# Optimization experiments

Measured on AMD Instinct MI355X. Metric: run time of the kernel, lower is better.

Reference implementation:

```python
import jax, jax.numpy as jnp
import numpy as np

GRID_SIZE = 5
G1 = GRID_SIZE + 1
GRID = jnp.linspace(-1.0, 1.0, G1)
INV2SIG2 = 0.5 * GRID_SIZE ** 2  # 1/(2*sigma^2), sigma = 1/grid_size
L = 3      # num_layers
NH = 8     # num_heads
C = 256    # feature_dim
HID = 1024 # hidden_dim


def kan(x, bw, sw):
    # x: (T, in), bw: (out, in), sw: (out, in, G1)
    base = x @ bw.T
    bases = jnp.exp(-((x[..., None] - GRID) ** 2) * INV2SIG2)  # (T, in, G1)
    bases = bases / (bases.sum(-1, keepdims=True) + 1e-8)
    return base + jnp.einsum('big,oig->bo', bases, sw)


def layernorm(x, g, b, eps=1e-5):
    m = x.mean(-1, keepdims=True)
    v = x.var(-1, keepdims=True)
    return (x - m) / jnp.sqrt(v + eps) * g + b


def gelu(x):
    return jax.nn.gelu(x, approximate=False)


def _forward(sat_features, uav_features,
             sat_qkvp_base, sat_qkvp_spline, sat_rp_base, sat_rp_spline,
             uav_qkvp_base, uav_qkvp_spline, uav_rp_base, uav_rp_spline,
             ref_w1_base, ref_w1_spline, ref_w2_base, ref_w2_spline, ref_ln_g, ref_ln_b,
             sim_w1_base, sim_w1_spline, sim_w2_base, sim_w2_spline, sim_w3_base, sim_w3_spline,
             fus_w_base, fus_w_spline, fus_ln_g, fus_ln_b):
    B, Cc, H, W = sat_features.shape
    N = H * W
    HD = Cc // NH
    scale = HD ** -0.5
    sat = sat_features.reshape(B, Cc, N).transpose(0, 2, 1)  # (B, N, C)
    uav = uav_features.reshape(B, Cc, N).transpose(0, 2, 1)

    # relative coords (same geometry every layer)
    ch = jnp.arange(H)
    cw = jnp.arange(W)
    coords = jnp.stack(jnp.meshgrid(ch, cw, indexing='ij')).reshape(2, N)  # (2, N)
    rel = (coords[:, :, None] - coords[:, None, :]).transpose(1, 2, 0).astype(jnp.float32)  # (N, N, 2)
    rel = rel / jnp.array([H - 1.0, W - 1.0], dtype=jnp.float32)
    rel_flat = rel.reshape(-1, 2)

    def attn_block(x, qb, qs, rb, rs):
        xf = x.reshape(-1, Cc)
        q = kan(xf, qb[0], qs[0]).reshape(B, N, NH, HD).transpose(0, 2, 1, 3)
        k = kan(xf, qb[1], qs[1]).reshape(B, N, NH, HD).transpose(0, 2, 1, 3)
        v = kan(xf, qb[2], qs[2]).reshape(B, N, NH, HD).transpose(0, 2, 1, 3)
        bias = kan(rel_flat, rb, rs).reshape(N, N, NH).transpose(2, 0, 1)  # (NH, N, N)
        a = jnp.einsum('bhnd,bhmd->bhnm', q, k) * scale + bias[None]
        a = jax.nn.softmax(a, axis=-1)
        o = jnp.einsum('bhnm,bhmd->bhnd', a, v).transpose(0, 2, 1, 3).reshape(B, N, Cc)
        return kan(o.reshape(-1, Cc), qb[3], qs[3]).reshape(B, N, Cc)

    def refine(x, i):
        xf = x.reshape(-1, Cc)
        h = gelu(kan(xf, ref_w1_base[i], ref_w1_spline[i]))
        h = kan(h, ref_w2_base[i], ref_w2_spline[i])
        h = layernorm(h, ref_ln_g[i], ref_ln_b[i])
        return h.reshape(x.shape)

    for i in range(L):
        se = attn_block(sat, sat_qkvp_base[i], sat_qkvp_spline[i], sat_rp_base[i], sat_rp_spline[i])
        ue = attn_block(uav, uav_qkvp_base[i], uav_qkvp_spline[i], uav_rp_base[i], uav_rp_spline[i])
        sat = se + refine(se, i)
        uav = ue + refine(ue, i)

    sg = sat.mean(1)  # (B, C)
    ug = uav.mean(1)
    si = jnp.concatenate([sg, ug], axis=1)
    h = gelu(kan(si, sim_w1_base, sim_w1_spline))
    h = gelu(kan(h, sim_w2_base, sim_w2_spline))
    w = jax.nn.sigmoid(kan(h, sim_w3_base, sim_w3_spline))  # (B, 1)
    fi = jnp.concatenate([sg * w, ug * (1.0 - w)], axis=1)
    out = gelu(layernorm(kan(fi, fus_w_base, fus_w_spline), fus_ln_g, fus_ln_b))
    return out


def setup_inputs() -> dict:
    key = jax.random.key(0)
    ks = jax.random.split(key, 32)
    B, H, W = 8, 24, 24
    n = lambda k, shape, s=0.05: jax.random.normal(k, shape, dtype=jnp.float32) * s
    inp = {
        'sat_features': jax.random.normal(ks[0], (B, C, H, W), dtype=jnp.float32),
        'uav_features': jax.random.normal(ks[1], (B, C, H, W), dtype=jnp.float32),
        'sat_qkvp_base': n(ks[2], (L, 4, C, C)),
        'sat_qkvp_spline': n(ks[3], (L, 4, C, C, G1), 0.01),
        'sat_rp_base': n(ks[4], (L, NH, 2)),
        'sat_rp_spline': n(ks[5], (L, NH, 2, G1), 0.01),
        'uav_qkvp_base': n(ks[6], (L, 4, C, C)),
        'uav_qkvp_spline': n(ks[7], (L, 4, C, C, G1), 0.01),
        'uav_rp_base': n(ks[8], (L, NH, 2)),
        'uav_rp_spline': n(ks[9], (L, NH, 2, G1), 0.01),
        'ref_w1_base': n(ks[10], (L, HID, C)),
        'ref_w1_spline': n(ks[11], (L, HID, C, G1), 0.01),
        'ref_w2_base': n(ks[12], (L, C, HID)),
        'ref_w2_spline': n(ks[13], (L, C, HID, G1), 0.01),
        'ref_ln_g': jnp.ones((L, C), jnp.float32),
        'ref_ln_b': jnp.zeros((L, C), jnp.float32),
        'sim_w1_base': n(ks[14], (HID, 2 * C)),
        'sim_w1_spline': n(ks[15], (HID, 2 * C, G1), 0.01),
        'sim_w2_base': n(ks[16], (C // 4, HID)),
        'sim_w2_spline': n(ks[17], (C // 4, HID, G1), 0.01),
        'sim_w3_base': n(ks[18], (1, C // 4)),
        'sim_w3_spline': n(ks[19], (1, C // 4, G1), 0.01),
        'fus_w_base': n(ks[20], (C, 2 * C)),
        'fus_w_spline': n(ks[21], (C, 2 * C, G1), 0.01),
        'fus_ln_g': jnp.ones((C,), jnp.float32),
        'fus_ln_b': jnp.zeros((C,), jnp.float32),
    }
    return inp


def reference(sat_features, uav_features,
              sat_qkvp_base, sat_qkvp_spline, sat_rp_base, sat_rp_spline,
              uav_qkvp_base, uav_qkvp_spline, uav_rp_base, uav_rp_spline,
              ref_w1_base, ref_w1_spline, ref_w2_base, ref_w2_spline, ref_ln_g, ref_ln_b,
              sim_w1_base, sim_w1_spline, sim_w2_base, sim_w2_spline, sim_w3_base, sim_w3_spline,
              fus_w_base, fus_w_spline, fus_ln_g, fus_ln_b):
    return _forward(sat_features, uav_features,
                    sat_qkvp_base, sat_qkvp_spline, sat_rp_base, sat_rp_spline,
                    uav_qkvp_base, uav_qkvp_spline, uav_rp_base, uav_rp_spline,
                    ref_w1_base, ref_w1_spline, ref_w2_base, ref_w2_spline, ref_ln_g, ref_ln_b,
                    sim_w1_base, sim_w1_spline, sim_w2_base, sim_w2_spline, sim_w3_base, sim_w3_spline,
                    fus_w_base, fus_w_spline, fus_ln_g, fus_ln_b)
```

## Files before the change

### kernel.cpp

```cpp
#include <hip/hip_runtime.h>
#include <math.h>

#define TT      4608
#define BB      8
#define NTOK    576
#define CDIM    256
#define NHEADS  8
#define HIDDIM  1024

typedef __attribute__((ext_vector_type(8))) short bf8s;
typedef __attribute__((ext_vector_type(4))) float f4;
typedef __attribute__((ext_vector_type(4))) short sv4;
typedef __attribute__((ext_vector_type(8))) short sv8;

__device__ __forceinline__ f4 mfma16(bf8s a, bf8s b, f4 c) {
    return __builtin_amdgcn_mfma_f32_16x16x32_bf16(a, b, c, 0, 0, 0);
}

__device__ __forceinline__ unsigned short f2bf(float x) {
    union { float f; unsigned int u; } v; v.f = x;
    unsigned int r = v.u + 0x7FFFu + ((v.u >> 16) & 1u);
    return (unsigned short)(r >> 16);
}
__device__ __forceinline__ float bf2f(unsigned short h) {
    union { unsigned int u; float f; } v; v.u = ((unsigned int)h) << 16;
    return v.f;
}
__device__ __forceinline__ unsigned int cvtpk(float a, float b) {
    unsigned int r;
    asm("v_cvt_pk_bf16_f32 %0, %1, %2" : "=v"(r) : "v"(a), "v"(b));
    return r;
}

__device__ __forceinline__ float gelu_f(float x) {
    return 0.5f * x * (1.0f + erff(x * 0.70710678118654752f));
}

__device__ __forceinline__ void bases6(float v, float* out) {
    float vc = fminf(fmaxf(v, -1.6f), 1.6f);
    float t = fmaf(vc, 10.f, 10.f);
    float r = __expf(t);
    float e0 = 1.f;
    float e1 = r * 1.3533528e-1f;
    float e2 = e1 * (r * 2.4787522e-3f);
    float e3 = e2 * (r * 4.5399930e-5f);
    float e4 = e3 * (r * 8.3152872e-7f);
    float e5 = e4 * (r * 1.5229979e-8f);
    float av = fmaxf(fabsf(v) - 1.f, 0.f);
    float g = __expf(fminf(fmaf(av * av, 12.5f, -18.420681f), 80.f));
    float inv = 1.f / ((e0 + e1 + e2 + e3 + e4 + e5) * (1.f + g));
    out[0] = e0 * inv; out[1] = e1 * inv; out[2] = e2 * inv;
    out[3] = e3 * inv; out[4] = e4 * inv; out[5] = e5 * inv;
}

__device__ __forceinline__ int4 expand_pack(float v) {
    float b6[6]; bases6(v, b6);
    int4 pk;
    pk.x = (int)cvtpk(v, b6[0]);
    pk.y = (int)cvtpk(b6[1], b6[2]);
    pk.z = (int)cvtpk(b6[3], b6[4]);
    pk.w = (int)cvtpk(b6[5], 0.f);
    return pk;
}

__device__ __forceinline__ void gload16(const void* g, void* l) {
    __builtin_amdgcn_global_load_lds(
        (const __attribute__((address_space(1))) unsigned int*)g,
        (__attribute__((address_space(3))) unsigned int*)l, 16, 0, 0);
}

__global__ __launch_bounds__(256) void k_transpose(const float* __restrict__ in,
                                                   float* __restrict__ out) {
    int idx = blockIdx.x * 256 + threadIdx.x;
    if (idx >= TT * CDIM) return;
    int t = idx >> 8, c = idx & 255;
    int b = t / NTOK, n = t % NTOK;
    out[idx] = in[(b * CDIM + c) * NTOK + n];
}

__global__ __launch_bounds__(256) void k_reduceS(const float4* __restrict__ p,
                                                 float4* __restrict__ out, int n4, int S) {
    int i = blockIdx.x * 256 + threadIdx.x;
    if (i >= n4) return;
    float4 a = p[i];
    for (int s = 1; s < S; s++) {
        float4 v = p[i + (size_t)s * n4];
        a.x += v.x; a.y += v.y; a.z += v.z; a.w += v.w;
    }
    out[i] = a;
}

__global__ __launch_bounds__(256) void k_reduce_exp(const float4* __restrict__ p,
                                                    float4* __restrict__ seb,
                                                    unsigned short* __restrict__ aexp,
                                                    int n4, int S) {
    int i = blockIdx.x * 256 + threadIdx.x;
    if (i >= n4) return;
    float4 a = p[i];
    for (int s = 1; s < S; s++) {
        float4 v = p[i + (size_t)s * n4];
        a.x += v.x; a.y += v.y; a.z += v.z; a.w += v.w;
    }
    seb[i] = a;
    int t = i >> 6, i4 = (i & 63) << 2;
    float xa[4] = {a.x, a.y, a.z, a.w};
#pragma unroll
    for (int u = 0; u < 4; u++) {
        int4 pk = expand_pack(xa[u]);
        *(int4*)(aexp + (size_t)t * 2048 + (size_t)(i4 + u) * 8) = pk;
    }
}

__global__ __launch_bounds__(256) void k_expand8(const float* __restrict__ x,
                                                 unsigned short* __restrict__ out, int Mr) {
    int idx = blockIdx.x * 256 + threadIdx.x;
    if (idx >= Mr * 64) return;
    int t = idx >> 6, i4 = (idx & 63) << 2;
    float4 xv = *(const float4*)(x + (size_t)t * 256 + i4);
    float xa[4] = {xv.x, xv.y, xv.z, xv.w};
#pragma unroll
    for (int u = 0; u < 4; u++) {
        int4 pk = expand_pack(xa[u]);
        *(int4*)(out + (size_t)t * 2048 + (size_t)(i4 + u) * 8) = pk;
    }
}

__global__ __launch_bounds__(256) void k_pack8(
    const float* __restrict__ sqb, const float* __restrict__ sqs,
    const float* __restrict__ uqb, const float* __restrict__ uqs,
    const float* __restrict__ w1b, const float* __restrict__ w1s,
    const float* __restrict__ w2b, const float* __restrict__ w2s,
    unsigned short* __restrict__ Wq, unsigned short* __restrict__ Wp,
    unsigned short* __restrict__ Ww1, unsigned short* __restrict__ Ww2) {
    const size_t gQ = 196608, gP = 65536, g1 = 262144;
    size_t idx = (size_t)blockIdx.x * 256 + threadIdx.x;
    const float* base; const float* spl; unsigned short* dst; size_t off;
    if (idx < 2 * gQ) {
        int s = idx >= gQ; off = idx - (size_t)s * gQ;
        base = s ? uqb : sqb; spl = s ? uqs : sqs; dst = Wq + (size_t)s * gQ * 8;
    } else if (idx < 2 * gQ + 2 * gP) {
        size_t o2 = idx - 2 * gQ; int s = o2 >= gP; off = o2 - (size_t)s * gP;
        base = (s ? uqb : sqb) + 3 * 65536; spl = (s ? uqs : sqs) + 3 * 393216;
        dst = Wp + (size_t)s * gP * 8;
    } else if (idx < 2 * gQ + 2 * gP + g1) {
        off = idx - 2 * gQ - 2 * gP; base = w1b; spl = w1s; dst = Ww1;
    } else {
        off = idx - 2 * gQ - 2 * gP - g1; base = w2b; spl = w2s; dst = Ww2;
    }
    float bv = base[off];
    float2 s01 = *(const float2*)(spl + off * 6);
    float2 s23 = *(const float2*)(spl + off * 6 + 2);
    float2 s45 = *(const float2*)(spl + off * 6 + 4);
    int4 pk;
    pk.x = (int)cvtpk(bv, s01.x);
    pk.y = (int)cvtpk(s01.y, s23.x);
    pk.z = (int)cvtpk(s23.y, s45.x);
    pk.w = (int)cvtpk(s45.y, 0.f);
    *(int4*)(dst + off * 8) = pk;
}

template<int BM, int BN, int ACT, int CMODE, int EXP>
__global__ __launch_bounds__(256) void mgemm(const void* __restrict__ Araw,
                                             const unsigned short* __restrict__ W0,
                                             const unsigned short* __restrict__ W1,
                                             void* __restrict__ Cv, int NN, int K,
                                             int ALD, int WLD, int gx, int groupRows,
                                             int S, int Kc, size_t skStride) {
    constexpr int MF = BM / 32;
    constexpr int NF = BN / 32;
    __shared__ unsigned short As[2][BM * 32];
    __shared__ unsigned short Bs[2][BN * 32];
    int nwg = gridDim.x, orig = blockIdx.x;
    int q = nwg >> 3, r = nwg & 7;
    int xcd = orig & 7, loc = orig >> 3;
    int wg = (xcd < r ? xcd * (q + 1) : r * (q + 1) + (xcd - r) * q) + loc;
    int sk = wg % S; int rest = wg / S;
    int bx = rest % gx, by = rest / gx;
    const int bm = by * BM, bn = bx * BN;
    const unsigned short* W = (bm >= groupRows) ? W1 : W0;
    const int tid = threadIdx.x, l = tid & 63, w = tid >> 6;
    const int wr = w >> 1, wc = w & 1;
    const int sr = l >> 2;
    const int scg = (l & 3) ^ ((l >> 3) & 3);
    const int sc8 = scg * 8;
    const int fro = (l & 15) * 32 + (((l >> 4) ^ ((l >> 1) & 3)) << 3);
    const int k0 = sk * Kc;
    f4 acc[MF][NF];
#pragma unroll
    for (int m = 0; m < MF; m++)
#pragma unroll
        for (int n = 0; n < NF; n++) acc[m][n] = (f4){0.f, 0.f, 0.f, 0.f};

    const unsigned short* Abf = (const unsigned short*)Araw;
    float xv[BM / 64];
    auto loadX = [&](int kt) {
#pragma unroll
        for (int it = 0; it < BM / 64; it++) {
            int ch = it * 4 + w;
            int row = bm + ch * 16 + sr;
            int xi = (kt >> 3) + scg;
            xv[it] = bf2f(Abf[(size_t)row * ALD + xi]);
        }
    };
    auto writeA = [&](int buf) {
#pragma unroll
        for (int it = 0; it < BM / 64; it++) {
            int ch = it * 4 + w;
            int4 pk = expand_pack(xv[it]);
            *(int4*)&As[buf][ch * 512 + l * 8] = pk;
        }
    };
    auto stageA = [&](int buf, int kt) {
#pragma unroll
        for (int it = 0; it < BM / 64; it++) {
            int ch = it * 4 + w;
            gload16(Abf + (size_t)(bm + ch * 16 + sr) * ALD + kt + sc8,
                    (void*)(&As[buf][ch * 512 + l * 8]));
        }
    };
    auto stageB = [&](int buf, int kt) {
#pragma unroll
        for (int it = 0; it < BN / 64; it++) {
            int ch = it * 4 + w;
            gload16(W + (size_t)(bn + ch * 16 + sr) * WLD + kt + sc8,
                    (void*)(&Bs[buf][ch * 512 + l * 8]));
        }
    };

    if constexpr (EXP == 0) stageA(0, k0);
    else { loadX(k0); writeA(0); }
    stageB(0, k0);
    __syncthreads();
    const int nt = Kc / 32;
    for (int t = 0; t < nt; t++) {
        int cur = t & 1;
        if (t + 1 < nt) {
            if constexpr (EXP == 0) stageA(cur ^ 1, k0 + (t + 1) * 32);
            else loadX(k0 + (t + 1) * 32);
            stageB(cur ^ 1, k0 + (t + 1) * 32);
        }
        bf8s af[MF], bfr[NF];
#pragma unroll
        for (int m = 0; m < MF; m++)
            af[m] = *(const bf8s*)&As[cur][(wr * MF + m) * 512 + fro];
#pragma unroll
        for (int n = 0; n < NF; n++)
            bfr[n] = *(const bf8s*)&Bs[cur][(wc * NF + n) * 512 + fro];
#pragma unroll
        for (int m = 0; m < MF; m++)
#pragma unroll
            for (int n = 0; n < NF; n++)
                acc[m][n] = mfma16(af[m], bfr[n], acc[m][n]);
        if constexpr (EXP != 0) { if (t + 1 < nt) writeA(cur ^ 1); }
        __syncthreads();
    }
#pragma unroll
    for (int m = 0; m < MF; m++)
#pragma unroll
        for (int n = 0; n < NF; n++)
#pragma unroll
            for (int j = 0; j < 4; j++) {
                int row = bm + wr * (BM / 2) + m * 16 + (l >> 4) * 4 + j;
                int col = bn + wc * (BN / 2) + n * 16 + (l & 15);
                float v = acc[m][n][j];
                if (ACT == 1) v = gelu_f(v);
                size_t o = (size_t)row * NN + col;
                if (CMODE == 0)      ((float*)Cv)[(size_t)sk * skStride + o] = v;
                else                 ((unsigned short*)Cv)[o] = f2bf(v);
            }
}

__global__ __launch_bounds__(256) void k_vt(const unsigned short* __restrict__ QKV,
                                            unsigned short* __restrict__ VT) {
    const int n0 = blockIdx.x * 64, h = blockIdx.y, z = blockIdx.z;
    __shared__ unsigned short t[32][72];
    const int tid = threadIdx.x;
    {
        int nl = tid >> 2, d8 = (tid & 3) * 8;
        sv8 v = *(const sv8*)(QKV + ((size_t)z * 576 + n0 + nl) * 768 + 512 + h * 32 + d8);
#pragma unroll
        for (int j = 0; j < 8; j++) t[d8 + j][nl] = v[j];
    }
    __syncthreads();
    {
        int d = tid >> 3, n8 = (tid & 7) * 8;
        sv8 o;
#pragma unroll
        for (int j = 0; j < 8; j++) o[j] = t[d][n8 + j];
        *(sv8*)(VT + ((size_t)(z * 8 + h) * 32 + d) * 576 + n0 + n8) = o;
    }
}

__global__ __launch_bounds__(256) void k_bias_tab(const float* __restrict__ rb0,
                                                  const float* __restrict__ rs0,
                                                  const float* __restrict__ rb1,
                                                  const float* __restrict__ rs1,
                                                  float* __restrict__ Btab) {
    int sidx = blockIdx.y;
    const float* rb = sidx ? rb1 : rb0;
    const float* rs = sidx ? rs1 : rs0;
    float* B = Btab + (size_t)sidx * NHEADS * 2209;
    int idx = blockIdx.x * 256 + threadIdx.x;
    if (idx >= 2209) return;
    float r0 = (float)(idx / 47 - 23) * (1.0f / 23.0f);
    float r1 = (float)(idx % 47 - 23) * (1.0f / 23.0f);
    float v[2][6];
    bases6(r0, v[0]);
    bases6(r1, v[1]);
#pragma unroll
    for (int h = 0; h < NHEADS; h++) {
        float s = rb[h * 2] * r0 + rb[h * 2 + 1] * r1;
#pragma unroll
        for (int g = 0; g < 6; g++)
            s += rs[h * 12 + g] * v[0][g] + rs[h * 12 + 6 + g] * v[1][g];
        B[(size_t)h * 2209 + idx] = s;
    }
}

__global__ __launch_bounds__(256) void k_attn2(const unsigned short* __restrict__ QKV,
                                               const unsigned short* __restrict__ VT,
                                               const float* __restrict__ Btab,
                                               unsigned short* __restrict__ AX) {
    int nwg = gridDim.x, orig = blockIdx.x;
    int qq = nwg >> 3, rr_ = nwg & 7;
    int xcd = orig & 7, loc = orig >> 3;
    int wg = (xcd < rr_ ? xcd * (qq + 1) : rr_ * (qq + 1) + (xcd - rr_) * qq) + loc;
    const int n0 = (wg % 18) * 32;
    const int h = (wg / 18) & 7;
    const int z = wg / 144;
    const int tid = threadIdx.x, l = tid & 63, w = tid >> 6;
    const int rh = (w & 1) * 16;
    const int kh = (w >> 1) * 16;
    __shared__ unsigned short Ps[4][32 * 40];
    __shared__ float red[4][16];
    __shared__ float bt[2209];
    const float scale = 0.17677669529663687f;
    const size_t rowbase = (size_t)z * NTOK;
    const float* Bh = Btab + ((size_t)(z >> 3) * NHEADS + h) * 2209;
    for (int i = tid; i < 2209; i += 256) bt[i] = Bh[i];
    const unsigned short* VTh = VT + ((size_t)(z * 8 + h) * 32) * 576;

    bf8s qf = *(const bf8s*)(QKV + (rowbase + n0 + rh + (l & 15)) * 768 + h * 32 + (l >> 4) * 8);

    f4 s[18];
#pragma unroll
    for (int kc = 0; kc < 18; kc++) {
        bf8s kf = *(const bf8s*)(QKV + (rowbase + kc * 32 + kh + (l & 15)) * 768 + 256 + h * 32 + (l >> 4) * 8);
        f4 zz = {0.f, 0.f, 0.f, 0.f};
        s[kc] = mfma16(qf, kf, zz);
    }
    __syncthreads();

    const int r0 = n0 + rh + (l >> 4) * 4;
    int bidx[4];
#pragma unroll
    for (int j = 0; j < 4; j++) {
        int n = r0 + j;
        bidx[j] = (n / 24 + 23) * 47 + (n % 24 + 23);
    }
    int m0 = kh + (l & 15);
    int mq = (m0 >= 24) ? 1 : 0;
    int mr = m0 - 24 * mq;
    float mx[4] = {-1e30f, -1e30f, -1e30f, -1e30f};
#pragma unroll
    for (int kc = 0; kc < 18; kc++) {
        int moff = mq * 47 + mr;
        mr += 8; mq += 1;
        if (mr >= 24) { mr -= 24; mq += 1; }
#pragma unroll
        for (int j = 0; j < 4; j++) {
            float v = s[kc][j] * scale + bt[bidx[j] - moff];
            s[kc][j] = v;
            mx[j] = fmaxf(mx[j], v);
        }
    }
#pragma unroll
    for (int j = 0; j < 4; j++)
#pragma unroll
        for (int m = 1; m < 16; m <<= 1) mx[j] = fmaxf(mx[j], __shfl_xor(mx[j], m));
    if ((l & 15) == 0) {
#pragma unroll
        for (int j = 0; j < 4; j++) red[w][(l >> 4) * 4 + j] = mx[j];
    }
    __syncthreads();
#pragma unroll
    for (int j = 0; j < 4; j++) mx[j] = fmaxf(mx[j], red[w ^ 2][(l >> 4) * 4 + j]);
    __syncthreads();
    float sm[4] = {0.f, 0.f, 0.f, 0.f};
#pragma unroll
    for (int kc = 0; kc < 18; kc++)
#pragma unroll
        for (int j = 0; j < 4; j++) {
            float p = __expf(s[kc][j] - mx[j]);
            s[kc][j] = p;
            sm[j] += p;
        }
#pragma unroll
    for (int j = 0; j < 4; j++)
#pragma unroll
        for (int m = 1; m < 16; m <<= 1) sm[j] += __shfl_xor(sm[j], m);
    if ((l & 15) == 0) {
#pragma unroll
        for (int j = 0; j < 4; j++) red[w][(l >> 4) * 4 + j] = sm[j];
    }
    __syncthreads();
#pragma unroll
    for (int j = 0; j < 4; j++) sm[j] = 1.f / (sm[j] + red[w ^ 2][(l >> 4) * 4 + j]);

    f4 oacc = {0.f, 0.f, 0.f, 0.f};
#pragma unroll
    for (int kc2 = 0; kc2 < 18; kc2 += 2) {
        const int b0 = kc2 & 2;
#pragma unroll
        for (int u = 0; u < 2; u++) {
            int kc = kc2 + u;
#pragma unroll
            for (int j = 0; j < 4; j++)
                Ps[b0 + u][(rh + (l >> 4) * 4 + j) * 40 + kh + (l & 15)] = f2bf(s[kc][j]);
        }
        __syncthreads();
#pragma unroll
        for (int u = 0; u < 2; u++) {
            int kc = kc2 + u;
            bf8s pf = *(const bf8s*)&Ps[b0 + u][(rh + (l & 15)) * 40 + (l >> 4) * 8];
            bf8s vf = *(const bf8s*)(VTh + (size_t)(kh + (l & 15)) * 576 + kc * 32 + (l >> 4) * 8);
            oacc = mfma16(pf, vf, oacc);
        }
    }
#pragma unroll
    for (int j = 0; j < 4; j++) {
        float ov = oacc[j] * sm[j];
        int4 pk = expand_pack(ov);
        *(int4*)(AX + ((rowbase + n0 + rh + (l >> 4) * 4 + j) * 2048
                       + (size_t)(h * 32 + kh + (l & 15)) * 8)) = pk;
    }
}

__global__ __launch_bounds__(256) void k_ln_addS(const float* __restrict__ P,
                                                 int S, size_t st,
                                                 const float* __restrict__ SE,
                                                 const float* __restrict__ g,
                                                 const float* __restrict__ bb,
                                                 float* __restrict__ Out,
                                                 unsigned short* __restrict__ aexp,
                                                 int doExp) {
    int t = blockIdx.x, c = threadIdx.x;
    size_t o = (size_t)t * 256 + c;
    float v = 0.f;
    for (int s = 0; s < S; s++) v += P[o + (size_t)s * st];
    float s1 = v, s2 = v * v;
#pragma unroll
    for (int off = 32; off; off >>= 1) { s1 += __shfl_xor(s1, off); s2 += __shfl_xor(s2, off); }
    __shared__ float p1[4], p2[4];
    int wv_ = c >> 6, ln = c & 63;
    if (ln == 0) { p1[wv_] = s1; p2[wv_] = s2; }
    __syncthreads();
    s1 = p1[0] + p1[1] + p1[2] + p1[3];
    s2 = p2[0] + p2[1] + p2[2] + p2[3];
    float m = s1 * (1.f / 256.f);
    float var = s2 * (1.f / 256.f) - m * m;
    float y = (v - m) * rsqrtf(var + 1e-5f) * g[c] + bb[c];
    float xn = SE[o] + y;
    Out[o] = xn;
    if (doExp) {
        int4 pk = expand_pack(xn);
        *(int4*)(aexp + (size_t)t * 2048 + (size_t)c * 8) = pk;
    }
}

__global__ __launch_bounds__(256) void k_ln_gelu(const float* __restrict__ Xin,
                                                 const float* __restrict__ g,
                                                 const float* __restrict__ bb,
                                                 float* __restrict__ Out) {
    int t = blockIdx.x, c = threadIdx.x;
    float v = Xin[t * 256 + c];
    float s1 = v, s2 = v * v;
#pragma unroll
    for (int off = 32; off; off >>= 1) { s1 += __shfl_xor(s1, off); s2 += __shfl_xor(s2, off); }
    __shared__ float p1[4], p2[4];
    int wv_ = c >> 6, ln = c & 63;
    if (ln == 0) { p1[wv_] = s1; p2[wv_] = s2; }
    __syncthreads();
    s1 = p1[0] + p1[1] + p1[2] + p1[3];
    s2 = p2[0] + p2[1] + p2[2] + p2[3];
    float m = s1 * (1.f / 256.f);
    float var = s2 * (1.f / 256.f) - m * m;
    float y = (v - m) * rsqrtf(var + 1e-5f) * g[c] + bb[c];
    Out[t * 256 + c] = gelu_f(y);
}

__global__ __launch_bounds__(256) void k_meanpool(const float* __restrict__ X,
                                                  float* __restrict__ si, int colofs) {
    int idx = blockIdx.x * 256 + threadIdx.x;
    if (idx >= BB * CDIM) return;
    int b = idx >> 8, c = idx & 255;
    float s = 0.f;
    for (int n = 0; n < NTOK; n++) s += X[(size_t)(b * NTOK + n) * CDIM + c];
    si[b * 512 + colofs + c] = s * (1.f / 576.f);
}

__global__ __launch_bounds__(256) void k_expand(const float* __restrict__ x,
                                                float* __restrict__ bases, int total) {
    int idx = blockIdx.x * 256 + threadIdx.x;
    if (idx >= total) return;
    float b6[6];
    bases6(x[idx], b6);
#pragma unroll
    for (int g = 0; g < 6; g++) bases[idx * 6 + g] = b6[g];
}

__global__ __launch_bounds__(64) void k_small_kan(const float* __restrict__ A1, int K1,
                                                  const float* __restrict__ A2, int K2,
                                                  const float* __restrict__ W1,
                                                  const float* __restrict__ W2,
                                                  float* __restrict__ out, int NN, int act) {
    int o = blockIdx.x, t = blockIdx.y, ln = threadIdx.x;
    float s = 0.f;
    for (int k = ln; k < K1; k += 64) s += A1[t * K1 + k] * W1[o * K1 + k];
    for (int k = ln; k < K2; k += 64) s += A2[t * K2 + k] * W2[o * K2 + k];
#pragma unroll
    for (int off = 32; off; off >>= 1) s += __shfl_xor(s, off);
    if (ln == 0) {
        if (act == 1) s = gelu_f(s);
        else if (act == 2) s = 1.f / (1.f + __expf(-s));
        out[t * NN + o] = s;
    }
}

__global__ void k_fi(const float* __restrict__ si, const float* __restrict__ wv,
                     float* __restrict__ fi) {
    int idx = blockIdx.x * 256 + threadIdx.x;
    if (idx >= BB * 512) return;
    int b = idx >> 9, i = idx & 511;
    float w = wv[b];
    fi[idx] = si[idx] * (i < 256 ? w : 1.f - w);
}

extern "C" void kernel_launch(void* const* d_in, const int* in_sizes, int n_in,
                              void* d_out, int out_size, void* d_ws, size_t ws_size,
                              hipStream_t stream) {
    (void)in_sizes; (void)n_in; (void)out_size;
    const float* sat_f = (const float*)d_in[0];
    const float* uav_f = (const float*)d_in[1];
    const float* s_qb  = (const float*)d_in[2];
    const float* s_qs  = (const float*)d_in[3];
    const float* s_rb  = (const float*)d_in[4];
    const float* s_rs  = (const float*)d_in[5];
    const float* u_qb  = (const float*)d_in[6];
    const float* u_qs  = (const float*)d_in[7];
    const float* u_rb  = (const float*)d_in[8];
    const float* u_rs  = (const float*)d_in[9];
    const float* r_w1b = (const float*)d_in[10];
    const float* r_w1s = (const float*)d_in[11];
    const float* r_w2b = (const float*)d_in[12];
    const float* r_w2s = (const float*)d_in[13];
    const float* r_lng = (const float*)d_in[14];
    const float* r_lnb = (const float*)d_in[15];
    const float* m_w1b = (const float*)d_in[16];
    const float* m_w1s = (const float*)d_in[17];
    const float* m_w2b = (const float*)d_in[18];
    const float* m_w2s = (const float*)d_in[19];
    const float* m_w3b = (const float*)d_in[20];
    const float* m_w3s = (const float*)d_in[21];
    const float* f_wb  = (const float*)d_in[22];
    const float* f_ws  = (const float*)d_in[23];
    const float* f_lng = (const float*)d_in[24];
    const float* f_lnb = (const float*)d_in[25];

    const size_t nQ = 1572864, nP = 524288;

    float* X; unsigned short* QKVb; unsigned short* VT; char* R; float* PS;
    unsigned short* AEXP;
    unsigned short *Wq, *Wp, *Ww1, *Ww2;
    float *Btab, *si, *SB, *h1f, *h2f, *wvv, *fiB, *ftmp;
    auto plan = [&](int nb, bool ded, bool assign) -> size_t {
        size_t off = 0;
        auto take = [&](size_t bytes) -> char* {
            char* rp = (char*)d_ws + off;
            off = (off + bytes + 255) & ~(size_t)255;
            return rp;
        };
        size_t Mr = (size_t)nb * TT;
        char* p;
        p = take((size_t)2 * TT * 256 * 4);             if (assign) X = (float*)p;
        p = take(Mr * 768 * 2);                         if (assign) QKVb = (unsigned short*)p;
        p = take(Mr * 256 * 2);                         if (assign) VT = (unsigned short*)p;
        p = take(Mr * 2048 * 2);                        if (assign) R = p;
        p = take((size_t)4 * Mr * 256 * 4);             if (assign) PS = (float*)p;
        if (ded) { p = take(Mr * 2048 * 2);             if (assign) AEXP = (unsigned short*)p; }
        else     { if (assign) AEXP = (unsigned short*)PS; }
        p = take(2 * nQ * 2);                           if (assign) Wq = (unsigned short*)p;
        p = take(2 * nP * 2);                           if (assign) Wp = (unsigned short*)p;
        p = take((size_t)2097152 * 2);                  if (assign) Ww1 = (unsigned short*)p;
        p = take((size_t)2097152 * 2);                  if (assign) Ww2 = (unsigned short*)p;
        p = take((size_t)nb * NHEADS * 2209 * 4);       if (assign) Btab = (float*)p;
        p = take(BB * 512 * 4);                         if (assign) si = (float*)p;
        p = take((size_t)BB * 1024 * 6 * 4);            if (assign) SB = (float*)p;
        p = take(BB * 1024 * 4);                        if (assign) h1f = (float*)p;
        p = take(BB * 64 * 4);                          if (assign) h2f = (float*)p;
        p = take(64 * 4);                               if (assign) wvv = (float*)p;
        p = take(BB * 512 * 4);                         if (assign) fiB = (float*)p;
        p = take(BB * 256 * 4);                         if (assign) ftmp = (float*)p;
        return off;
    };
    int nb; bool ded;
    if      (ws_size >= plan(2, true,  false)) { nb = 2; ded = true;  }
    else if (ws_size >= plan(2, false, false)) { nb = 2; ded = false; }
    else                                       { nb = 1; ded = true;  }
    plan(nb, ded, true);
    const bool fuseRed = ded;
    const bool fuseLn  = ded && (nb == 2);

    k_transpose<<<TT, 256, 0, stream>>>(sat_f, X);
    k_transpose<<<TT, 256, 0, stream>>>(uav_f, X + (size_t)TT * 256);

    const int Mr = nb * TT;
    const size_t pStride = (size_t)Mr * 256;
    unsigned short* AEXPp = (unsigned short*)R;
    unsigned short* H1bp  = (unsigned short*)R;
    float* SEbp = (float*)(R + (size_t)Mr * 1024 * 2);

    for (int l = 0; l < 3; l++) {
        k_pack8<<<4096, 256, 0, stream>>>(
            s_qb + (size_t)l * 262144, s_qs + (size_t)l * 1572864,
            u_qb + (size_t)l * 262144, u_qs + (size_t)l * 1572864,
            r_w1b + (size_t)l * 262144, r_w1s + (size_t)l * 1572864,
            r_w2b + (size_t)l * 262144, r_w2s + (size_t)l * 1572864,
            Wq, Wp, Ww1, Ww2);

        for (int st0 = 0; st0 < 2; st0 += nb) {
            float* Xs = X + (size_t)st0 * TT * 256;
            bool haveAexp = fuseLn && (l > 0);
            if (!haveAexp) k_expand8<<<Mr / 4, 256, 0, stream>>>(Xs, AEXP, Mr);
            mgemm<128, 128, 0, 2, 0><<<6 * (Mr / 128), 256, 0, stream>>>(
                AEXP, Wq + (size_t)st0 * nQ, Wq + nQ, (void*)QKVb, 768, 2048, 2048, 2048, 6, TT, 1, 2048, 0);
            k_vt<<<dim3(9, 8, nb * 8), 256, 0, stream>>>(QKVb, VT);
            {
                const float* rbA = (st0 ? u_rb : s_rb) + l * 16;
                const float* rsA = (st0 ? u_rs : s_rs) + l * 96;
                k_bias_tab<<<dim3(9, nb), 256, 0, stream>>>(rbA, rsA, u_rb + l * 16, u_rs + l * 96, Btab);
            }
            k_attn2<<<144 * nb * 8, 256, 0, stream>>>(QKVb, VT, Btab, AEXPp);
            mgemm<128, 128, 0, 0, 0><<<2 * (Mr / 128) * 2, 256, 0, stream>>>(
                AEXPp, Wp + (size_t)st0 * nP, Wp + nP, (void*)PS, 256, 2048, 2048, 2048, 2, TT, 2, 1024, pStride);
            if (fuseRed)
                k_reduce_exp<<<Mr / 4, 256, 0, stream>>>((const float4*)PS, (float4*)SEbp, AEXP, Mr * 64, 2);
            else {
                k_reduceS<<<Mr / 4, 256, 0, stream>>>((const float4*)PS, (float4*)SEbp, Mr * 64, 2);
                k_expand8<<<Mr / 4, 256, 0, stream>>>(SEbp, AEXP, Mr);
            }
            mgemm<128, 128, 1, 2, 0><<<8 * (Mr / 128), 256, 0, stream>>>(
                AEXP, Ww1, Ww1, (void*)H1bp, 1024, 2048, 2048, 2048, 8, TT, 1, 2048, 0);
            mgemm<64, 256, 0, 0, 2><<<4 * (Mr / 64), 256, 0, stream>>>(
                H1bp, Ww2, Ww2, (void*)PS, 256, 8192, 1024, 8192, 1, TT, 4, 2048, pStride);
            k_ln_addS<<<Mr, 256, 0, stream>>>(PS, 4, pStride, SEbp,
                                              r_lng + l * 256, r_lnb + l * 256, Xs,
                                              AEXP, (fuseLn && l < 2) ? 1 : 0);
        }
    }

    k_meanpool<<<8, 256, 0, stream>>>(X, si, 0);
    k_meanpool<<<8, 256, 0, stream>>>(X + (size_t)TT * 256, si, 256);
    k_expand<<<(BB * 512 + 255) / 256, 256, 0, stream>>>(si, SB, BB * 512);
    k_small_kan<<<dim3(1024, BB), 64, 0, stream>>>(si, 512, SB, 3072, m_w1b, m_w1s, h1f, 1024, 1);
    k_expand<<<(BB * 1024 + 255) / 256, 256, 0, stream>>>(h1f, SB, BB * 1024);
    k_small_kan<<<dim3(64, BB), 64, 0, stream>>>(h1f, 1024, SB, 6144, m_w2b, m_w2s, h2f, 64, 1);
    k_expand<<<(BB * 64 + 255) / 256, 256, 0, stream>>>(h2f, SB, BB * 64);
    k_small_kan<<<dim3(1, BB), 64, 0, stream>>>(h2f, 64, SB, 384, m_w3b, m_w3s, wvv, 1, 2);
    k_fi<<<16, 256, 0, stream>>>(si, wvv, fiB);
    k_expand<<<(BB * 512 + 255) / 256, 256, 0, stream>>>(fiB, SB, BB * 512);
    k_small_kan<<<dim3(256, BB), 64, 0, stream>>>(fiB, 512, SB, 3072, f_wb, f_ws, ftmp, 256, 0);
    k_ln_gelu<<<8, 256, 0, stream>>>(ftmp, f_lng, f_lnb, (float*)d_out);
}
```

Measured before the change: 1.103 ms.

## Fuse V transpose into QKV GEMM epilogue, pack all layers once, raise split-K

The QKV GEMM gains an epilogue mode that writes the V columns straight into the transposed VT layout, which removes the separate k_vt kernel and its round trip through QKV. Weight packing for all three layers now runs in a single launch before the layer loop when the workspace allows. Split-K factors also rise, from 2 to 4 for the projection GEMM and from 4 to 8 for the W2 GEMM, so these GEMMs fill more CUs at the price of more partial sums to reduce. The workspace plan adds fallback tiers for these options, and the VT stores are 4-element strided writes that may coalesce poorly.

```diff
diff --git a/kernel.cpp b/kernel.cpp
--- a/kernel.cpp
+++ b/kernel.cpp
@@ -133,19 +133,25 @@
     unsigned short* __restrict__ Wq, unsigned short* __restrict__ Wp,
     unsigned short* __restrict__ Ww1, unsigned short* __restrict__ Ww2) {
     const size_t gQ = 196608, gP = 65536, g1 = 262144;
+    const int ly = blockIdx.y;
+    const size_t bofs = (size_t)ly * 262144, sofs = (size_t)ly * 1572864;
     size_t idx = (size_t)blockIdx.x * 256 + threadIdx.x;
     const float* base; const float* spl; unsigned short* dst; size_t off;
     if (idx < 2 * gQ) {
         int s = idx >= gQ; off = idx - (size_t)s * gQ;
-        base = s ? uqb : sqb; spl = s ? uqs : sqs; dst = Wq + (size_t)s * gQ * 8;
+        base = (s ? uqb : sqb) + bofs; spl = (s ? uqs : sqs) + sofs;
+        dst = Wq + (size_t)ly * 3145728 + (size_t)s * gQ * 8;
     } else if (idx < 2 * gQ + 2 * gP) {
         size_t o2 = idx - 2 * gQ; int s = o2 >= gP; off = o2 - (size_t)s * gP;
-        base = (s ? uqb : sqb) + 3 * 65536; spl = (s ? uqs : sqs) + 3 * 393216;
-        dst = Wp + (size_t)s * gP * 8;
+        base = (s ? uqb : sqb) + bofs + 3 * 65536;
+        spl  = (s ? uqs : sqs) + sofs + 3 * 393216;
+        dst = Wp + (size_t)ly * 1048576 + (size_t)s * gP * 8;
     } else if (idx < 2 * gQ + 2 * gP + g1) {
-        off = idx - 2 * gQ - 2 * gP; base = w1b; spl = w1s; dst = Ww1;
+        off = idx - 2 * gQ - 2 * gP;
+        base = w1b + bofs; spl = w1s + sofs; dst = Ww1 + (size_t)ly * 2097152;
     } else {
-        off = idx - 2 * gQ - 2 * gP - g1; base = w2b; spl = w2s; dst = Ww2;
+        off = idx - 2 * gQ - 2 * gP - g1;
+        base = w2b + bofs; spl = w2s + sofs; dst = Ww2 + (size_t)ly * 2097152;
     }
     float bv = base[off];
     float2 s01 = *(const float2*)(spl + off * 6);
@@ -163,7 +169,9 @@
 __global__ __launch_bounds__(256) void mgemm(const void* __restrict__ Araw,
                                              const unsigned short* __restrict__ W0,
                                              const unsigned short* __restrict__ W1,
-                                             void* __restrict__ Cv, int NN, int K,
+                                             void* __restrict__ Cv,
+                                             unsigned short* __restrict__ VTp,
+                                             int NN, int K,
                                              int ALD, int WLD, int gx, int groupRows,
                                              int S, int Kc, size_t skStride) {
     constexpr int MF = BM / 32;
@@ -257,38 +265,28 @@
 #pragma unroll
     for (int m = 0; m < MF; m++)
 #pragma unroll
-        for (int n = 0; n < NF; n++)
-#pragma unroll
-            for (int j = 0; j < 4; j++) {
-                int row = bm + wr * (BM / 2) + m * 16 + (l >> 4) * 4 + j;
-                int col = bn + wc * (BN / 2) + n * 16 + (l & 15);
-                float v = acc[m][n][j];
-                if (ACT == 1) v = gelu_f(v);
-                size_t o = (size_t)row * NN + col;
-                if (CMODE == 0)      ((float*)Cv)[(size_t)sk * skStride + o] = v;
-                else                 ((unsigned short*)Cv)[o] = f2bf(v);
+        for (int n = 0; n < NF; n++) {
+            int row0 = bm + wr * (BM / 2) + m * 16 + (l >> 4) * 4;
+            int col = bn + wc * (BN / 2) + n * 16 + (l & 15);
+            if (CMODE == 4 && col >= 512) {
+                int hh = (col - 512) >> 5, dd = (col - 512) & 31;
+                int z = ((row0 >> 6) * 57) >> 9;
+                int nv = row0 - z * 576;
+                sv4 o;
+#pragma unroll
+                for (int j = 0; j < 4; j++) o[j] = (short)f2bf(acc[m][n][j]);
+                *(sv4*)(VTp + ((size_t)(z * 8 + hh) * 32 + dd) * 576 + nv) = o;
+            } else {
+#pragma unroll
+                for (int j = 0; j < 4; j++) {
+                    float v = acc[m][n][j];
+                    if (ACT == 1) v = gelu_f(v);
+                    size_t o = (size_t)(row0 + j) * NN + col;
+                    if (CMODE == 0)      ((float*)Cv)[(size_t)sk * skStride + o] = v;
+                    else                 ((unsigned short*)Cv)[o] = f2bf(v);
+                }
             }
-}
-
-__global__ __launch_bounds__(256) void k_vt(const unsigned short* __restrict__ QKV,
-                                            unsigned short* __restrict__ VT) {
-    const int n0 = blockIdx.x * 64, h = blockIdx.y, z = blockIdx.z;
-    __shared__ unsigned short t[32][72];
-    const int tid = threadIdx.x;
-    {
-        int nl = tid >> 2, d8 = (tid & 3) * 8;
-        sv8 v = *(const sv8*)(QKV + ((size_t)z * 576 + n0 + nl) * 768 + 512 + h * 32 + d8);
-#pragma unroll
-        for (int j = 0; j < 8; j++) t[d8 + j][nl] = v[j];
-    }
-    __syncthreads();
-    {
-        int d = tid >> 3, n8 = (tid & 7) * 8;
-        sv8 o;
-#pragma unroll
-        for (int j = 0; j < 8; j++) o[j] = t[d][n8 + j];
-        *(sv8*)(VT + ((size_t)(z * 8 + h) * 32 + d) * 576 + n0 + n8) = o;
-    }
+        }
 }
 
 __global__ __launch_bounds__(256) void k_bias_tab(const float* __restrict__ rb0,
@@ -573,7 +571,7 @@
     unsigned short* AEXP;
     unsigned short *Wq, *Wp, *Ww1, *Ww2;
     float *Btab, *si, *SB, *h1f, *h2f, *wvv, *fiB, *ftmp;
-    auto plan = [&](int nb, bool ded, bool assign) -> size_t {
+    auto plan = [&](int nb, bool ded, bool pall, int sw2, bool assign) -> size_t {
         size_t off = 0;
         auto take = [&](size_t bytes) -> char* {
             char* rp = (char*)d_ws + off;
@@ -581,18 +579,20 @@
             return rp;
         };
         size_t Mr = (size_t)nb * TT;
+        int nl = pall ? 3 : 1;
         char* p;
         p = take((size_t)2 * TT * 256 * 4);             if (assign) X = (float*)p;
         p = take(Mr * 768 * 2);                         if (assign) QKVb = (unsigned short*)p;
         p = take(Mr * 256 * 2);                         if (assign) VT = (unsigned short*)p;
         p = take(Mr * 2048 * 2);                        if (assign) R = p;
-        p = take((size_t)4 * Mr * 256 * 4);             if (assign) PS = (float*)p;
+        size_t psSlices = (size_t)(sw2 > 4 ? sw2 : 4);
+        p = take(psSlices * Mr * 256 * 4);              if (assign) PS = (float*)p;
         if (ded) { p = take(Mr * 2048 * 2);             if (assign) AEXP = (unsigned short*)p; }
         else     { if (assign) AEXP = (unsigned short*)PS; }
-        p = take(2 * nQ * 2);                           if (assign) Wq = (unsigned short*)p;
-        p = take(2 * nP * 2);                           if (assign) Wp = (unsigned short*)p;
-        p = take((size_t)2097152 * 2);                  if (assign) Ww1 = (unsigned short*)p;
-        p = take((size_t)2097152 * 2);                  if (assign) Ww2 = (unsigned short*)p;
+        p = take((size_t)nl * 2 * nQ * 2);              if (assign) Wq = (unsigned short*)p;
+        p = take((size_t)nl * 2 * nP * 2);              if (assign) Wp = (unsigned short*)p;
+        p = take((size_t)nl * 2097152 * 2);             if (assign) Ww1 = (unsigned short*)p;
+        p = take((size_t)nl * 2097152 * 2);             if (assign) Ww2 = (unsigned short*)p;
         p = take((size_t)nb * NHEADS * 2209 * 4);       if (assign) Btab = (float*)p;
         p = take(BB * 512 * 4);                         if (assign) si = (float*)p;
         p = take((size_t)BB * 1024 * 6 * 4);            if (assign) SB = (float*)p;
@@ -603,11 +603,13 @@
         p = take(BB * 256 * 4);                         if (assign) ftmp = (float*)p;
         return off;
     };
-    int nb; bool ded;
-    if      (ws_size >= plan(2, true,  false)) { nb = 2; ded = true;  }
-    else if (ws_size >= plan(2, false, false)) { nb = 2; ded = false; }
-    else                                       { nb = 1; ded = true;  }
-    plan(nb, ded, true);
+    int nb; bool ded, pall; int SW2;
+    if      (ws_size >= plan(2, true,  true,  8, false)) { nb = 2; ded = true;  pall = true;  SW2 = 8; }
+    else if (ws_size >= plan(2, true,  false, 8, false)) { nb = 2; ded = true;  pall = false; SW2 = 8; }
+    else if (ws_size >= plan(2, true,  false, 4, false)) { nb = 2; ded = true;  pall = false; SW2 = 4; }
+    else if (ws_size >= plan(2, false, false, 4, false)) { nb = 2; ded = false; pall = false; SW2 = 4; }
+    else                                                 { nb = 1; ded = true;  pall = false; SW2 = 8; }
+    plan(nb, ded, pall, SW2, true);
     const bool fuseRed = ded;
     const bool fuseLn  = ded && (nb == 2);
 
@@ -620,40 +622,53 @@
     unsigned short* H1bp  = (unsigned short*)R;
     float* SEbp = (float*)(R + (size_t)Mr * 1024 * 2);
 
+    if (pall)
+        k_pack8<<<dim3(4096, 3), 256, 0, stream>>>(s_qb, s_qs, u_qb, u_qs,
+                                                   r_w1b, r_w1s, r_w2b, r_w2s,
+                                                   Wq, Wp, Ww1, Ww2);
+
     for (int l = 0; l < 3; l++) {
-        k_pack8<<<4096, 256, 0, stream>>>(
-            s_qb + (size_t)l * 262144, s_qs + (size_t)l * 1572864,
-            u_qb + (size_t)l * 262144, u_qs + (size_t)l * 1572864,
-            r_w1b + (size_t)l * 262144, r_w1s + (size_t)l * 1572864,
-            r_w2b + (size_t)l * 262144, r_w2s + (size_t)l * 1572864,
-            Wq, Wp, Ww1, Ww2);
+        if (!pall)
+            k_pack8<<<dim3(4096, 1), 256, 0, stream>>>(
+                s_qb + (size_t)l * 262144, s_qs + (size_t)l * 1572864,
+                u_qb + (size_t)l * 262144, u_qs + (size_t)l * 1572864,
+                r_w1b + (size_t)l * 262144, r_w1s + (size_t)l * 1572864,
+                r_w2b + (size_t)l * 262144, r_w2s + (size_t)l * 1572864,
+                Wq, Wp, Ww1, Ww2);
+        unsigned short* WqL  = Wq  + (pall ? (size_t)l * 2 * nQ : 0);
+        unsigned short* WpL  = Wp  + (pall ? (size_t)l * 2 * nP : 0);
+        unsigned short* Ww1L = Ww1 + (pall ? (size_t)l * 2097152 : 0);
+        unsigned short* Ww2L = Ww2 + (pall ? (size_t)l * 2097152 : 0);
 
         for (int st0 = 0; st0 < 2; st0 += nb) {
             float* Xs = X + (size_t)st0 * TT * 256;
             bool haveAexp = fuseLn && (l > 0);
             if (!haveAexp) k_expand8<<<Mr / 4, 256, 0, stream>>>(Xs, AEXP, Mr);
-            mgemm<128, 128, 0, 2, 0><<<6 * (Mr / 128), 256, 0, stream>>>(
-                AEXP, Wq + (size_t)st0 * nQ, Wq + nQ, (void*)QKVb, 768, 2048, 2048, 2048, 6, TT, 1, 2048, 0);
-            k_vt<<<dim3(9, 8, nb * 8), 256, 0, stream>>>(QKVb, VT);
+            mgemm<128, 128, 0, 4, 0><<<6 * (Mr / 128), 256, 0, stream>>>(
+                AEXP, WqL + (size_t)st0 * nQ, WqL + nQ, (void*)QKVb, VT,
+                768, 2048, 2048, 2048, 6, TT, 1, 2048, 0);
             {
                 const float* rbA = (st0 ? u_rb : s_rb) + l * 16;
                 const float* rsA = (st0 ? u_rs : s_rs) + l * 96;
                 k_bias_tab<<<dim3(9, nb), 256, 0, stream>>>(rbA, rsA, u_rb + l * 16, u_rs + l * 96, Btab);
             }
             k_attn2<<<144 * nb * 8, 256, 0, stream>>>(QKVb, VT, Btab, AEXPp);
-            mgemm<128, 128, 0, 0, 0><<<2 * (Mr / 128) * 2, 256, 0, stream>>>(
-                AEXPp, Wp + (size_t)st0 * nP, Wp + nP, (void*)PS, 256, 2048, 2048, 2048, 2, TT, 2, 1024, pStride);
+            mgemm<128, 128, 0, 0, 0><<<2 * (Mr / 128) * 4, 256, 0, stream>>>(
+                AEXPp, WpL + (size_t)st0 * nP, WpL + nP, (void*)PS, nullptr,
+                256, 2048, 2048, 2048, 2, TT, 4, 512, pStride);
             if (fuseRed)
-                k_reduce_exp<<<Mr / 4, 256, 0, stream>>>((const float4*)PS, (float4*)SEbp, AEXP, Mr * 64, 2);
+                k_reduce_exp<<<Mr / 4, 256, 0, stream>>>((const float4*)PS, (float4*)SEbp, AEXP, Mr * 64, 4);
             else {
-                k_reduceS<<<Mr / 4, 256, 0, stream>>>((const float4*)PS, (float4*)SEbp, Mr * 64, 2);
+                k_reduceS<<<Mr / 4, 256, 0, stream>>>((const float4*)PS, (float4*)SEbp, Mr * 64, 4);
                 k_expand8<<<Mr / 4, 256, 0, stream>>>(SEbp, AEXP, Mr);
             }
             mgemm<128, 128, 1, 2, 0><<<8 * (Mr / 128), 256, 0, stream>>>(
-                AEXP, Ww1, Ww1, (void*)H1bp, 1024, 2048, 2048, 2048, 8, TT, 1, 2048, 0);
-            mgemm<64, 256, 0, 0, 2><<<4 * (Mr / 64), 256, 0, stream>>>(
-                H1bp, Ww2, Ww2, (void*)PS, 256, 8192, 1024, 8192, 1, TT, 4, 2048, pStride);
-            k_ln_addS<<<Mr, 256, 0, stream>>>(PS, 4, pStride, SEbp,
+                AEXP, Ww1L, Ww1L, (void*)H1bp, nullptr,
+                1024, 2048, 2048, 2048, 8, TT, 1, 2048, 0);
+            mgemm<64, 256, 0, 0, 2><<<SW2 * (Mr / 64), 256, 0, stream>>>(
+                H1bp, Ww2L, Ww2L, (void*)PS, nullptr,
+                256, 8192, 1024, 8192, 1, TT, SW2, 8192 / SW2, pStride);
+            k_ln_addS<<<Mr, 256, 0, stream>>>(PS, SW2, pStride, SEbp,
                                               r_lng + l * 256, r_lnb + l * 256, Xs,
                                               AEXP, (fuseLn && l < 2) ? 1 : 0);
         }
```

Result: slower. 1.148 ms (+4.1%).
